# Optimization experiments

Measured on AMD Instinct MI355X. Metric: run time of the kernel, lower is better.

## Reference

```python
import jax, jax.numpy as jnp
import numpy as np

EMBED_DIM = 2048
N_HEADS = 16
N_KV_HEADS = 4
HEAD_DIM = EMBED_DIM // N_HEADS  # 128
NUM_REP = N_HEADS // N_KV_HEADS  # 4
BATCH = 4
SEQLEN = 2048


def setup_inputs() -> dict:
    key = jax.random.key(0)
    kx, kq, kk, kv, ko = jax.random.split(key, 5)
    x = jax.random.normal(kx, (BATCH, SEQLEN, EMBED_DIM), dtype=jnp.float32)
    # Real RoPE table (theta=10000), shape (seqlen, head_dim//2)
    inv_freq = 1.0 / (10000.0 ** (jnp.arange(0, HEAD_DIM, 2, dtype=jnp.float32) / HEAD_DIM))
    t = jnp.arange(SEQLEN, dtype=jnp.float32)
    ang = jnp.outer(t, inv_freq)  # (S, hd/2)
    freqs_cos = jnp.cos(ang)
    freqs_sin = jnp.sin(ang)
    std = 0.02
    wq = jax.random.normal(kq, (EMBED_DIM, N_HEADS * HEAD_DIM), dtype=jnp.float32) * std
    wk = jax.random.normal(kk, (EMBED_DIM, N_KV_HEADS * HEAD_DIM), dtype=jnp.float32) * std
    wv = jax.random.normal(kv, (EMBED_DIM, N_KV_HEADS * HEAD_DIM), dtype=jnp.float32) * std
    wo = jax.random.normal(ko, (N_HEADS * HEAD_DIM, EMBED_DIM), dtype=jnp.float32) * std
    return {"x": x, "freqs_cos": freqs_cos, "freqs_sin": freqs_sin,
            "wq": wq, "wk": wk, "wv": wv, "wo": wo}


def _apply_rope(xh, cos, sin):
    # xh: (b, s, h, hd); cos/sin: (s, hd/2) -> broadcast (1, s, 1, hd/2)
    b, s, h, hd = xh.shape
    xr = xh.reshape(b, s, h, hd // 2, 2)
    x0, x1 = xr[..., 0], xr[..., 1]  # real/imag of complex pairs
    c = cos[None, :, None, :]
    sn = sin[None, :, None, :]
    o0 = x0 * c - x1 * sn
    o1 = x0 * sn + x1 * c
    return jnp.stack([o0, o1], axis=-1).reshape(b, s, h, hd)


def reference(x, freqs_cos, freqs_sin, wq, wk, wv, wo):
    bs, s, _ = x.shape
    xq = (x @ wq).reshape(bs, s, N_HEADS, HEAD_DIM)
    xk = (x @ wk).reshape(bs, s, N_KV_HEADS, HEAD_DIM)
    xv = (x @ wv).reshape(bs, s, N_KV_HEADS, HEAD_DIM)
    xq = _apply_rope(xq, freqs_cos, freqs_sin)
    xk = _apply_rope(xk, freqs_cos, freqs_sin)
    # repeat_kv (GQA): interleave-repeat kv heads to match query heads
    keys = jnp.repeat(xk, NUM_REP, axis=2)    # (b, s, H, hd)
    values = jnp.repeat(xv, NUM_REP, axis=2)
    scale = 1.0 / jnp.sqrt(jnp.float32(HEAD_DIM))
    # SDPA, non-causal
    scores = jnp.einsum('bqhd,bkhd->bhqk', xq, keys) * scale
    probs = jax.nn.softmax(scores, axis=-1)
    out = jnp.einsum('bhqk,bkhd->bqhd', probs, values)
    out = out.reshape(bs, s, N_HEADS * HEAD_DIM)
    return out @ wo
```

## Files before the change

### kernel.cpp

```cpp
#include <hip/hip_runtime.h>
#include <stdint.h>


typedef unsigned short u16;
typedef __bf16 bf16x8 __attribute__((ext_vector_type(8)));
typedef float  f32x4  __attribute__((ext_vector_type(4)));
typedef unsigned int u32x2 __attribute__((ext_vector_type(2)));

#define GLOAD16(gp, lp)                                                        \
  __builtin_amdgcn_global_load_lds(                                            \
      (const __attribute__((address_space(1))) void*)(gp),                     \
      (__attribute__((address_space(3))) void*)(lp), 16, 0, 0)

__device__ __forceinline__ u16 f2b(float f) {
  union { float f; uint32_t u; } v; v.f = f;
  uint32_t r = v.u + 0x7FFFu + ((v.u >> 16) & 1u);
  return (u16)(r >> 16);
}
__device__ __forceinline__ float b2f(u16 h) {
  union { uint32_t u; float f; } v; v.u = ((uint32_t)h) << 16;
  return v.f;
}
__device__ __forceinline__ uint2 pack4(float a, float b, float c, float d) {
  uint2 r;
  asm("v_cvt_pk_bf16_f32 %0, %1, %2" : "=v"(r.x) : "v"(a), "v"(b));
  asm("v_cvt_pk_bf16_f32 %0, %1, %2" : "=v"(r.y) : "v"(c), "v"(d));
  return r;
}

__device__ __forceinline__ void bar_sync() {
  asm volatile("s_waitcnt lgkmcnt(0)" ::: "memory");
  __builtin_amdgcn_s_barrier();
  asm volatile("" ::: "memory");
}

__global__ __launch_bounds__(256) void cast_x_kernel(const float4* __restrict__ in,
                                                     ushort4* __restrict__ out) {
  int i = blockIdx.x * 256 + threadIdx.x;
  float4 v = in[i];
  ushort4 o;
  o.x = f2b(v.x); o.y = f2b(v.y); o.z = f2b(v.z); o.w = f2b(v.w);
  out[i] = o;
}

__global__ __launch_bounds__(256) void wtrans_kernel(const float* __restrict__ W,
                                                     u16* __restrict__ WT,
                                                     int K, int N, float scale) {
  __shared__ float t[32][33];
  int n0 = blockIdx.x * 32, k0 = blockIdx.y * 32;
  int tx = threadIdx.x, ty = threadIdx.y;
  for (int r = 0; r < 4; r++)
    t[ty + r * 8][tx] = W[(size_t)(k0 + ty + r * 8) * N + n0 + tx];
  __syncthreads();
  for (int r = 0; r < 4; r++)
    WT[(size_t)(n0 + ty + r * 8) * K + k0 + tx] = f2b(t[tx][ty + r * 8] * scale);
}

template <bool BF16OUT>
__global__ __launch_bounds__(256) void gemm_bt_kernel(const u16* __restrict__ A,
                                                      const u16* __restrict__ BT,
                                                      void* __restrict__ Cv,
                                                      int K, int N) {
  __shared__ u16 As[128 * 64];
  __shared__ u16 Bs[128 * 64];
  const int tid = threadIdx.x;
  const int wave = tid >> 6, lane = tid & 63;
  const int quad = lane >> 4, l16 = lane & 15;
  const int wm = (wave >> 1) * 64, wn = (wave & 1) * 64;
  const size_t m0 = (size_t)blockIdx.y * 128, n0 = (size_t)blockIdx.x * 128;

  f32x4 acc[4][4] = {};
  const int srow = lane >> 3;
  const int scol = ((lane & 7) ^ srow) * 8;
  const u16* Ag = A + (m0 + wave * 8 + srow) * (size_t)K + scol;
  const u16* Bg = BT + (n0 + wave * 8 + srow) * (size_t)K + scol;
  const int sw7 = l16 & 7;

  for (int k0 = 0; k0 < K; k0 += 64) {
    for (int c = 0; c < 4; c++) {
      GLOAD16(Ag + (size_t)(c * 32) * K + k0, &As[(c * 32 + wave * 8) * 64]);
      GLOAD16(Bg + (size_t)(c * 32) * K + k0, &Bs[(c * 32 + wave * 8) * 64]);
    }
    __syncthreads();
    for (int kk = 0; kk < 2; kk++) {
      bf16x8 af[4], bf[4];
      const int ch = ((4 * kk + quad) ^ sw7) << 3;
      for (int i = 0; i < 4; i++)
        af[i] = *(const bf16x8*)&As[(wm + i * 16 + l16) * 64 + ch];
      for (int i = 0; i < 4; i++)
        bf[i] = *(const bf16x8*)&Bs[(wn + i * 16 + l16) * 64 + ch];
      for (int mi = 0; mi < 4; mi++)
        for (int ni = 0; ni < 4; ni++)
          acc[mi][ni] = __builtin_amdgcn_mfma_f32_16x16x32_bf16(af[mi], bf[ni], acc[mi][ni], 0, 0, 0);
    }
    __syncthreads();
  }
  for (int mi = 0; mi < 4; mi++)
    for (int ni = 0; ni < 4; ni++)
      for (int r = 0; r < 4; r++) {
        size_t row = m0 + wm + mi * 16 + quad * 4 + r;
        size_t col = n0 + wn + ni * 16 + l16;
        if (BF16OUT) ((u16*)Cv)[row * N + col] = f2b(acc[mi][ni][r]);
        else         ((float*)Cv)[row * N + col] = acc[mi][ni][r];
      }
}

__global__ __launch_bounds__(256) void rope_kernel(u16* __restrict__ QKV,
                                                   const float* __restrict__ cs,
                                                   const float* __restrict__ sn) {
  int tid = blockIdx.x * 256 + threadIdx.x;
  int row = tid / 1280;
  int p = tid - row * 1280;
  int s = row & 2047;
  int head = p >> 6, i = p & 63;
  u16* ptr = QKV + (size_t)row * 3072 + head * 128 + i * 2;
  unsigned int v = *(unsigned int*)ptr;
  float x0 = b2f((u16)(v & 0xffff)), x1 = b2f((u16)(v >> 16));
  float c = cs[s * 64 + i], ss = sn[s * 64 + i];
  u16 o0 = f2b(x0 * c - x1 * ss);
  u16 o1 = f2b(x0 * ss + x1 * c);
  *(unsigned int*)ptr = (unsigned int)o0 | ((unsigned int)o1 << 16);
}

__global__ __launch_bounds__(256) void vtrans_kernel(const u16* __restrict__ QKV,
                                                     u16* __restrict__ Vt) {
  __shared__ u16 t[32][33];
  int b = blockIdx.z >> 2, hk = blockIdx.z & 3;
  int s0 = blockIdx.x * 32, d0 = blockIdx.y * 32;
  int tx = threadIdx.x, ty = threadIdx.y;
  const u16* src = QKV + (size_t)(b * 2048 + s0) * 3072 + 2560 + hk * 128 + d0;
  for (int r = 0; r < 4; r++)
    t[ty + r * 8][tx] = src[(size_t)(ty + r * 8) * 3072 + tx];
  __syncthreads();
  u16* dst = Vt + ((size_t)((b * 4 + hk) * 128 + d0)) * 2048 + s0;
  for (int r = 0; r < 4; r++)
    dst[(size_t)(ty + r * 8) * 2048 + tx] = t[tx][ty + r * 8];
}

__global__ __launch_bounds__(256, 2) void attn_kernel(const u16* __restrict__ QKV,
                                                      const u16* __restrict__ Vt,
                                                      u16* __restrict__ AO) {
  __shared__ u16 KP[128 * 128];
  __shared__ u16 Vls[128 * 128];
  const int tid = threadIdx.x;
  const int wave = tid >> 6, lane = tid & 63;
  const int quad = lane >> 4, l16 = lane & 15;
  const int qt = blockIdx.x, h = blockIdx.y, b = blockIdx.z;
  const int hk = h >> 2;
  const int sw = l16 & 7;

  bf16x8 qf[2][4];
  {
    const u16* Qb = QKV + (size_t)(b * 2048 + qt * 128 + wave * 32) * 3072 + h * 128;
    for (int qb = 0; qb < 2; qb++)
      for (int ki = 0; ki < 4; ki++)
        qf[qb][ki] = *(const bf16x8*)(Qb + (size_t)(qb * 16 + l16) * 3072 + ki * 32 + quad * 8);
  }
  f32x4 o[8][2] = {};
  float m_[2] = {-1e30f, -1e30f}, l_[2] = {0.f, 0.f};

  const u16* Kg0 = QKV + 2048 + hk * 128;
  const u16* Vg0 = Vt + (size_t)((b * 4 + hk) * 128) * 2048;
  const int r4 = lane >> 4, c16 = lane & 15;

  auto stageK = [&](int t) {
    const u16* Kg = Kg0 + (size_t)(b * 2048 + t * 128) * 3072;
    for (int i = 0; i < 8; i++) {
      int grp = i * 4 + wave;
      int row = grp * 4 + r4;
      int ch = c16 ^ (row & 7);
      GLOAD16(Kg + (size_t)row * 3072 + ch * 8, &KP[grp * 512]);
    }
  };
  auto stageV = [&](int t) {
    const u16* Vg = Vg0 + t * 128;
    for (int i = 0; i < 8; i++) {
      int grp = i * 4 + wave;
      int row = grp * 4 + r4;
      int ch = c16 ^ (row & 7);
      GLOAD16(Vg + (size_t)row * 2048 + ch * 8, &Vls[grp * 512]);
    }
  };

  stageK(0);
  stageV(0);
  __syncthreads();

  for (int kt = 0; kt < 16; kt++) {
    if (kt > 0) stageV(kt);

    f32x4 s[8][2];
    for (int kb = 0; kb < 8; kb++) {
      bf16x8 kf[4];
      int a0 = (kb * 16 + l16) * 128 + ((quad ^ sw) << 3);
      for (int ki = 0; ki < 4; ki++)
        kf[ki] = *(const bf16x8*)&KP[a0 ^ (ki * 32)];
      __builtin_amdgcn_s_setprio(1);
      for (int qb = 0; qb < 2; qb++) {
        f32x4 a = {0.f, 0.f, 0.f, 0.f};
        for (int ki = 0; ki < 4; ki++)
          a = __builtin_amdgcn_mfma_f32_16x16x32_bf16(kf[ki], qf[qb][ki], a, 0, 0, 0);
        s[kb][qb] = a;
      }
      __builtin_amdgcn_s_setprio(0);
    }

    bar_sync();
    if (kt < 15) stageK(kt + 1);

    bf16x8 pf[2][4];
    float alch[2];
    for (int qb = 0; qb < 2; qb++) {
      float mk[8];
#pragma unroll
      for (int kb = 0; kb < 8; kb++)
        mk[kb] = fmaxf(fmaxf(s[kb][qb][0], s[kb][qb][1]),
                       fmaxf(s[kb][qb][2], s[kb][qb][3]));
      float mx = fmaxf(fmaxf(fmaxf(mk[0], mk[1]), fmaxf(mk[2], mk[3])),
                       fmaxf(fmaxf(mk[4], mk[5]), fmaxf(mk[6], mk[7])));
      mx = fmaxf(mx, __shfl_xor(mx, 16, 64));
      mx = fmaxf(mx, __shfl_xor(mx, 32, 64));
      float mn = m_[qb], al = 1.0f;
      if (!__all(mx <= m_[qb] + 8.0f)) {
        mn = fmaxf(m_[qb], mx);
        al = exp2f(m_[qb] - mn);
        m_[qb] = mn;
      }
      alch[qb] = al;
      uint2 u[8];
      float rs = 0.f;
#pragma unroll
      for (int kb = 0; kb < 8; kb++) {
        float p0 = exp2f(s[kb][qb][0] - mn), p1 = exp2f(s[kb][qb][1] - mn);
        float p2 = exp2f(s[kb][qb][2] - mn), p3 = exp2f(s[kb][qb][3] - mn);
        u[kb] = pack4(p0, p1, p2, p3);
        rs += (p0 + p1) + (p2 + p3);
      }
      rs += __shfl_xor(rs, 16, 64);
      rs += __shfl_xor(rs, 32, 64);
      l_[qb] = l_[qb] * al + rs;
      const bool qo = (quad & 1) != 0;
#pragma unroll
      for (int ki = 0; ki < 4; ki++) {
        u32x2 r1 = __builtin_amdgcn_permlane32_swap(u[2 * ki].x, u[2 * ki + 1].x, false, false);
        u32x2 r2 = __builtin_amdgcn_permlane32_swap(u[2 * ki].y, u[2 * ki + 1].y, false, false);
        uint32_t t1b = (uint32_t)__shfl_xor((int)r1[1], 16, 64);
        uint32_t t1a = (uint32_t)__shfl_xor((int)r1[0], 16, 64);
        uint32_t t2b = (uint32_t)__shfl_xor((int)r2[1], 16, 64);
        uint32_t t2a = (uint32_t)__shfl_xor((int)r2[0], 16, 64);
        uint4 d;
        d.x = qo ? t1b : (uint32_t)r1[0];
        d.y = qo ? t2b : (uint32_t)r2[0];
        d.z = qo ? (uint32_t)r1[1] : t1a;
        d.w = qo ? (uint32_t)r2[1] : t2a;
        pf[qb][ki] = *(bf16x8*)&d;
      }
    }
    if (alch[0] != 1.0f || alch[1] != 1.0f) {
#pragma unroll
      for (int db = 0; db < 8; db++) {
        o[db][0] *= alch[0];
        o[db][1] *= alch[1];
      }
    }

    if (kt == 15) asm volatile("s_waitcnt vmcnt(0)" ::: "memory");
    else          asm volatile("s_waitcnt vmcnt(8)" ::: "memory");
    bar_sync();

    for (int db = 0; db < 8; db++) {
      bf16x8 vf[4];
      int a0 = (db * 16 + l16) * 128 + ((quad ^ sw) << 3);
      for (int ki = 0; ki < 4; ki++)
        vf[ki] = *(const bf16x8*)&Vls[a0 ^ (ki * 32)];
      __builtin_amdgcn_s_setprio(1);
      for (int qb = 0; qb < 2; qb++)
        for (int ki = 0; ki < 4; ki++)
          o[db][qb] = __builtin_amdgcn_mfma_f32_16x16x32_bf16(vf[ki], pf[qb][ki], o[db][qb], 0, 0, 0);
      __builtin_amdgcn_s_setprio(0);
    }

    asm volatile("s_waitcnt vmcnt(0)" ::: "memory");
    bar_sync();
  }

  float inv[2] = {1.0f / l_[0], 1.0f / l_[1]};
  for (int qb = 0; qb < 2; qb++) {
    int rq = wave * 32 + qb * 16 + l16;
    for (int db = 0; db < 8; db++) {
      int ch = (db * 2 + (quad >> 1)) ^ sw;
      uint2 pv = pack4(o[db][qb][0] * inv[qb], o[db][qb][1] * inv[qb],
                       o[db][qb][2] * inv[qb], o[db][qb][3] * inv[qb]);
      *(uint2*)&KP[rq * 128 + (ch << 3) + (quad & 1) * 4] = pv;
    }
  }
  __syncthreads();
  u16* Ab = AO + (size_t)(b * 2048 + qt * 128) * 2048 + h * 128;
  for (int i = 0; i < 8; i++) {
    int row = i * 16 + (tid >> 4);
    int seg = tid & 15;
    int pc = seg ^ (row & 7);
    *(uint4*)(Ab + (size_t)row * 2048 + seg * 8) = *(const uint4*)&KP[row * 128 + pc * 8];
  }
}

extern "C" void kernel_launch(void* const* d_in, const int* in_sizes, int n_in,
                              void* d_out, int out_size, void* d_ws, size_t ws_size,
                              hipStream_t stream) {
  (void)in_sizes; (void)n_in; (void)out_size; (void)ws_size;
  const float* x    = (const float*)d_in[0];
  const float* fcos = (const float*)d_in[1];
  const float* fsin = (const float*)d_in[2];
  const float* wq   = (const float*)d_in[3];
  const float* wk   = (const float*)d_in[4];
  const float* wv   = (const float*)d_in[5];
  const float* wo   = (const float*)d_in[6];

  char* w = (char*)d_ws;
  u16* xb  = (u16*)w;
  u16* wT  = (u16*)(w + 33554432);
  u16* woT = (u16*)(w + 33554432 + 12582912);
  u16* QKV = (u16*)(w + 33554432 + 12582912 + 8388608);
  u16* Vt  = (u16*)(w + 33554432 + 12582912 + 8388608 + 50331648);
  u16* AO  = xb;

  const float C = 0.08838834764831845f * 1.44269504088896340f;

  cast_x_kernel<<<16384, 256, 0, stream>>>((const float4*)x, (ushort4*)xb);
  wtrans_kernel<<<dim3(64, 64), dim3(32, 8), 0, stream>>>(wq, wT, 2048, 2048, C);
  wtrans_kernel<<<dim3(16, 64), dim3(32, 8), 0, stream>>>(wk, wT + (size_t)2048 * 2048, 2048, 512, 1.0f);
  wtrans_kernel<<<dim3(16, 64), dim3(32, 8), 0, stream>>>(wv, wT + (size_t)2560 * 2048, 2048, 512, 1.0f);
  wtrans_kernel<<<dim3(64, 64), dim3(32, 8), 0, stream>>>(wo, woT, 2048, 2048, 1.0f);

  gemm_bt_kernel<true><<<dim3(24, 64), 256, 0, stream>>>(xb, wT, QKV, 2048, 3072);
  rope_kernel<<<40960, 256, 0, stream>>>(QKV, fcos, fsin);
  vtrans_kernel<<<dim3(64, 4, 16), dim3(32, 8), 0, stream>>>(QKV, Vt);
  attn_kernel<<<dim3(16, 16, 4), 256, 0, stream>>>(QKV, Vt, AO);
  gemm_bt_kernel<false><<<dim3(16, 64), 256, 0, stream>>>(AO, woT, (float*)d_out, 2048, 2048);
}
```

Measured before the change: 575.7 us.

## Double-buffer GEMM LDS tiles and remap workgroups across XCDs

The GEMM main loop is rebuilt around K=32 steps with two LDS buffers, so the next tile's global-to-LDS loads are issued before the MFMAs on the current tile. This needs only one barrier per step instead of two. It uses a new swizzled LDS layout, and raises wave priority with s_setprio around the MFMA block. Both the GEMM and attention kernels now remap linear block IDs so that neighbouring tiles land on the same XCD, aiming to improve L2 reuse. The risks are added register pressure, smaller K tiles meaning more barriers overall, and reliance on a bar_sync helper defined elsewhere.

Result: no change. 573.1 us (-0.5%).

```diff
diff --git a/kernel.cpp b/kernel.cpp
--- a/kernel.cpp
+++ b/kernel.cpp
@@ -56,45 +56,68 @@
     WT[(size_t)(n0 + ty + r * 8) * K + k0 + tx] = f2b(t[tx][ty + r * 8] * scale);
 }
 
+#define KSTEP(CUR, NXT, TT)                                                    \
+  {                                                                            \
+    asm volatile("s_waitcnt vmcnt(0)" ::: "memory");                           \
+    bar_sync();                                                                \
+    if ((TT) + 1 < nt) {                                                       \
+      const size_t k0 = (size_t)((TT) + 1) * 32;                               \
+      GLOAD16(Ag + k0, &As[NXT][ldst]);                                        \
+      GLOAD16(Ag + k0 + (size_t)16 * K, &As[NXT][ldst + 512]);                 \
+      GLOAD16(Bg + k0, &Bs[NXT][ldst]);                                        \
+      GLOAD16(Bg + k0 + (size_t)16 * K, &Bs[NXT][ldst + 512]);                 \
+    }                                                                          \
+    bf16x8 af[4], bf[4];                                                       \
+    for (int i = 0; i < 4; i++)                                                \
+      af[i] = *(const bf16x8*)&As[CUR][wm * 32 + i * 512 + lrd];               \
+    for (int i = 0; i < 4; i++)                                                \
+      bf[i] = *(const bf16x8*)&Bs[CUR][wn * 32 + i * 512 + lrd];               \
+    __builtin_amdgcn_s_setprio(1);                                             \
+    for (int mi = 0; mi < 4; mi++)                                             \
+      for (int ni = 0; ni < 4; ni++)                                           \
+        acc[mi][ni] = __builtin_amdgcn_mfma_f32_16x16x32_bf16(                 \
+            af[mi], bf[ni], acc[mi][ni], 0, 0, 0);                             \
+    __builtin_amdgcn_s_setprio(0);                                             \
+  }
+
 template <bool BF16OUT>
 __global__ __launch_bounds__(256) void gemm_bt_kernel(const u16* __restrict__ A,
                                                       const u16* __restrict__ BT,
                                                       void* __restrict__ Cv,
                                                       int K, int N) {
-  __shared__ u16 As[128 * 64];
-  __shared__ u16 Bs[128 * 64];
+  __shared__ u16 As[2][64 * 64];
+  __shared__ u16 Bs[2][64 * 64];
   const int tid = threadIdx.x;
   const int wave = tid >> 6, lane = tid & 63;
   const int quad = lane >> 4, l16 = lane & 15;
   const int wm = (wave >> 1) * 64, wn = (wave & 1) * 64;
-  const size_t m0 = (size_t)blockIdx.y * 128, n0 = (size_t)blockIdx.x * 128;
+
+  const int nbx = gridDim.x;
+  const int nwg = nbx * gridDim.y;
+  const int d = blockIdx.x + blockIdx.y * nbx;
+  const int w = (d & 7) * (nwg >> 3) + (d >> 3);
+  const size_t m0 = (size_t)(w / nbx) * 128, n0 = (size_t)(w % nbx) * 128;
 
   f32x4 acc[4][4] = {};
-  const int srow = lane >> 3;
-  const int scol = ((lane & 7) ^ srow) * 8;
-  const u16* Ag = A + (m0 + wave * 8 + srow) * (size_t)K + scol;
-  const u16* Bg = BT + (n0 + wave * 8 + srow) * (size_t)K + scol;
-  const int sw7 = l16 & 7;
-
-  for (int k0 = 0; k0 < K; k0 += 64) {
-    for (int c = 0; c < 4; c++) {
-      GLOAD16(Ag + (size_t)(c * 32) * K + k0, &As[(c * 32 + wave * 8) * 64]);
-      GLOAD16(Bg + (size_t)(c * 32) * K + k0, &Bs[(c * 32 + wave * 8) * 64]);
-    }
-    __syncthreads();
-    for (int kk = 0; kk < 2; kk++) {
-      bf16x8 af[4], bf[4];
-      const int ch = ((4 * kk + quad) ^ sw7) << 3;
-      for (int i = 0; i < 4; i++)
-        af[i] = *(const bf16x8*)&As[(wm + i * 16 + l16) * 64 + ch];
-      for (int i = 0; i < 4; i++)
-        bf[i] = *(const bf16x8*)&Bs[(wn + i * 16 + l16) * 64 + ch];
-      for (int mi = 0; mi < 4; mi++)
-        for (int ni = 0; ni < 4; ni++)
-          acc[mi][ni] = __builtin_amdgcn_mfma_f32_16x16x32_bf16(af[mi], bf[ni], acc[mi][ni], 0, 0, 0);
-    }
-    __syncthreads();
-  }
+  const int srow = wave * 32 + ((lane >> 3) << 1) + ((lane >> 2) & 1);
+  const int tcol = ((lane & 3) ^ ((lane >> 3) & 3)) * 8;
+  const u16* Ag = A + (m0 + srow) * (size_t)K + tcol;
+  const u16* Bg = BT + (n0 + srow) * (size_t)K + tcol;
+  const int ldst = wave * 1024;
+  const int lrd = (l16 >> 1) * 64 + (l16 & 1) * 32 +
+                  ((quad ^ ((l16 >> 1) & 3)) << 3);
+  const int nt = K >> 5;
+
+  GLOAD16(Ag, &As[0][ldst]);
+  GLOAD16(Ag + (size_t)16 * K, &As[0][ldst + 512]);
+  GLOAD16(Bg, &Bs[0][ldst]);
+  GLOAD16(Bg + (size_t)16 * K, &Bs[0][ldst + 512]);
+
+  for (int t = 0; t < nt; t += 2) {
+    KSTEP(0, 1, t);
+    KSTEP(1, 0, t + 1);
+  }
+
   for (int mi = 0; mi < 4; mi++)
     for (int ni = 0; ni < 4; ni++)
       for (int r = 0; r < 4; r++) {
@@ -145,7 +168,9 @@
   const int tid = threadIdx.x;
   const int wave = tid >> 6, lane = tid & 63;
   const int quad = lane >> 4, l16 = lane & 15;
-  const int qt = blockIdx.x, h = blockIdx.y, b = blockIdx.z;
+  const int d0s = blockIdx.x + 16 * (blockIdx.y + 16 * blockIdx.z);
+  const int w0 = (d0s & 7) * 128 + (d0s >> 3);
+  const int qt = w0 & 15, h = (w0 >> 4) & 15, b = w0 >> 8;
   const int hk = h >> 2;
   const int sw = l16 & 7;
 
```

## Rewrite GEMM as 256x256 double-buffered pipelined kernel and fuse RoPE epilogue

Applied to the files above, without the earlier changes.

Replaces the 128x128 single-buffered GEMM with a 512-thread 256x256 tile kernel that double-buffers LDS across 128-wide K steps. Global-to-LDS loads are interleaved with MFMA phases using barriers, vmcnt waits and s_setprio, and workgroups are remapped in an XCD-aware order. RoPE is fused into the QKV GEMM epilogue using a lane shuffle to fetch the pair element, which drops the separate rope kernel and its extra pass over QKV. The cost is larger LDS use, one workgroup per CU, and fewer workgroups (384 and 256) to fill the device.

New measurement: 1.619 ms. +181.3%, slower.

```diff
diff --git a/kernel.cpp b/kernel.cpp
--- a/kernel.cpp
+++ b/kernel.cpp
@@ -56,70 +56,131 @@
     WT[(size_t)(n0 + ty + r * 8) * K + k0 + tx] = f2b(t[tx][ty + r * 8] * scale);
 }
 
+#define STG_A(T, KS)                                                           \
+  GLOAD16(PA + (size_t)(T) * 64 + (KS) * 32,                                   \
+          &SH[(((T) & 1) * 2 + (KS)) * 8192 + ldw]);                           \
+  GLOAD16(PA + (size_t)128 * K + (size_t)(T) * 64 + (KS) * 32,                 \
+          &SH[(((T) & 1) * 2 + (KS)) * 8192 + ldw + 4096]);
+
+#define STG_B(T, KS)                                                           \
+  GLOAD16(PB + (size_t)(T) * 64 + (KS) * 32,                                   \
+          &SH[32768 + (((T) & 1) * 2 + (KS)) * 8192 + ldw]);                   \
+  GLOAD16(PB + (size_t)128 * K + (size_t)(T) * 64 + (KS) * 32,                 \
+          &SH[32768 + (((T) & 1) * 2 + (KS)) * 8192 + ldw + 4096]);
+
+#define PHASE(TP, KS, MH, STAGE_STMT, WAIT_STMT)                               \
+  {                                                                            \
+    bf16x8 af[4];                                                              \
+    const int ao = ((TP) * 2 + (KS)) * 8192;                                   \
+    for (int q = 0; q < 4; q++)                                                \
+      af[q] = *(const bf16x8*)&SH[ao + aBase + ((MH) * 4 + q) * 512];          \
+    if ((MH) == 0)                                                             \
+      for (int q = 0; q < 4; q++)                                              \
+        bf[q] = *(const bf16x8*)&SH[32768 + ao + bBase + q * 512];             \
+    STAGE_STMT;                                                                \
+    __builtin_amdgcn_s_barrier();                                              \
+    asm volatile("s_waitcnt lgkmcnt(0)" ::: "memory");                         \
+    __builtin_amdgcn_s_setprio(1);                                             \
+    for (int q = 0; q < 4; q++)                                                \
+      for (int nr = 0; nr < 4; nr++)                                           \
+        acc[(MH) * 4 + q][nr] = __builtin_amdgcn_mfma_f32_16x16x32_bf16(       \
+            af[q], bf[nr], acc[(MH) * 4 + q][nr], 0, 0, 0);                    \
+    __builtin_amdgcn_s_setprio(0);                                             \
+    WAIT_STMT;                                                                 \
+    __builtin_amdgcn_s_barrier();                                              \
+    asm volatile("" ::: "memory");                                             \
+  }
+
 template <bool BF16OUT>
-__global__ __launch_bounds__(256) void gemm_bt_kernel(const u16* __restrict__ A,
-                                                      const u16* __restrict__ BT,
-                                                      void* __restrict__ Cv,
-                                                      int K, int N) {
-  __shared__ u16 As[128 * 64];
-  __shared__ u16 Bs[128 * 64];
+__global__ __launch_bounds__(512, 1) void gemm_bt_kernel(const u16* __restrict__ A,
+                                                         const u16* __restrict__ BT,
+                                                         void* __restrict__ Cv,
+                                                         int K, int N,
+                                                         const float* __restrict__ cs,
+                                                         const float* __restrict__ sn) {
+  __shared__ u16 SH[65536];
   const int tid = threadIdx.x;
   const int wave = tid >> 6, lane = tid & 63;
   const int quad = lane >> 4, l16 = lane & 15;
-  const int wm = (wave >> 1) * 64, wn = (wave & 1) * 64;
-  const size_t m0 = (size_t)blockIdx.y * 128, n0 = (size_t)blockIdx.x * 128;
-
-  f32x4 acc[4][4] = {};
-  const int srow = lane >> 3;
-  const int scol = ((lane & 7) ^ srow) * 8;
-  const u16* Ag = A + (m0 + wave * 8 + srow) * (size_t)K + scol;
-  const u16* Bg = BT + (n0 + wave * 8 + srow) * (size_t)K + scol;
-  const int sw7 = l16 & 7;
-
-  for (int k0 = 0; k0 < K; k0 += 64) {
-    for (int c = 0; c < 4; c++) {
-      GLOAD16(Ag + (size_t)(c * 32) * K + k0, &As[(c * 32 + wave * 8) * 64]);
-      GLOAD16(Bg + (size_t)(c * 32) * K + k0, &Bs[(c * 32 + wave * 8) * 64]);
-    }
-    __syncthreads();
-    for (int kk = 0; kk < 2; kk++) {
-      bf16x8 af[4], bf[4];
-      const int ch = ((4 * kk + quad) ^ sw7) << 3;
-      for (int i = 0; i < 4; i++)
-        af[i] = *(const bf16x8*)&As[(wm + i * 16 + l16) * 64 + ch];
-      for (int i = 0; i < 4; i++)
-        bf[i] = *(const bf16x8*)&Bs[(wn + i * 16 + l16) * 64 + ch];
-      for (int mi = 0; mi < 4; mi++)
-        for (int ni = 0; ni < 4; ni++)
-          acc[mi][ni] = __builtin_amdgcn_mfma_f32_16x16x32_bf16(af[mi], bf[ni], acc[mi][ni], 0, 0, 0);
-    }
-    __syncthreads();
-  }
-  for (int mi = 0; mi < 4; mi++)
-    for (int ni = 0; ni < 4; ni++)
-      for (int r = 0; r < 4; r++) {
-        size_t row = m0 + wm + mi * 16 + quad * 4 + r;
-        size_t col = n0 + wn + ni * 16 + l16;
-        if (BF16OUT) ((u16*)Cv)[row * N + col] = f2b(acc[mi][ni][r]);
-        else         ((float*)Cv)[row * N + col] = acc[mi][ni][r];
-      }
-}
-
-__global__ __launch_bounds__(256) void rope_kernel(u16* __restrict__ QKV,
-                                                   const float* __restrict__ cs,
-                                                   const float* __restrict__ sn) {
-  int tid = blockIdx.x * 256 + threadIdx.x;
-  int row = tid / 1280;
-  int p = tid - row * 1280;
-  int s = row & 2047;
-  int head = p >> 6, i = p & 63;
-  u16* ptr = QKV + (size_t)row * 3072 + head * 128 + i * 2;
-  unsigned int v = *(unsigned int*)ptr;
-  float x0 = b2f((u16)(v & 0xffff)), x1 = b2f((u16)(v >> 16));
-  float c = cs[s * 64 + i], ss = sn[s * 64 + i];
-  u16 o0 = f2b(x0 * c - x1 * ss);
-  u16 o1 = f2b(x0 * ss + x1 * c);
-  *(unsigned int*)ptr = (unsigned int)o0 | ((unsigned int)o1 << 16);
+  const int wr = wave >> 2, wc = wave & 3;
+
+  const int nbx = gridDim.x;
+  const int nwg = nbx * gridDim.y;
+  const int d = blockIdx.x + blockIdx.y * nbx;
+  const int w = (d & 7) * (nwg >> 3) + (d >> 3);
+  const size_t m0 = (size_t)(w / nbx) * 256, n0 = (size_t)(w % nbx) * 256;
+
+  f32x4 acc[8][4] = {};
+
+  const int csw = ((lane & 3) ^ ((lane >> 2) & 3)) * 8;
+  const u16* PA = A + (m0 + wave * 16 + (lane >> 2)) * (size_t)K + csw;
+  const u16* PB = BT + (n0 + wave * 16 + (lane >> 2)) * (size_t)K + csw;
+  const int slot8 = (quad ^ (l16 & 3)) << 3;
+  const int aBase = (wr * 128 + l16) * 32 + slot8;
+  const int bBase = (wc * 64 + l16) * 32 + slot8;
+  const int ldw = wave * 512;
+
+  const int niter = K >> 7;
+
+  STG_A(0, 0) STG_A(0, 1) STG_B(0, 0) STG_B(0, 1)
+  STG_A(1, 0) STG_A(1, 1) STG_B(1, 0) STG_B(1, 1)
+  __syncthreads();
+
+  for (int i = 0; i < niter; i++) {
+    const int t0 = 2 * i;
+    const bool nx = (i + 1 < niter);
+    const bool p0 = (i > 0);
+    bf16x8 bf[4];
+    PHASE(0, 0, 0, if (p0) { STG_A(t0 + 1, 1) }, )
+    PHASE(0, 0, 1, if (p0) { STG_B(t0 + 1, 1) }, )
+    PHASE(0, 1, 0, if (nx) { STG_A(t0 + 2, 0) }, )
+    PHASE(0, 1, 1, if (nx) { STG_B(t0 + 2, 0) },
+          if (nx) { asm volatile("s_waitcnt vmcnt(4)" ::: "memory"); }
+          else    { asm volatile("s_waitcnt vmcnt(0)" ::: "memory"); })
+    PHASE(1, 0, 0, if (nx) { STG_A(t0 + 2, 1) }, )
+    PHASE(1, 0, 1, if (nx) { STG_B(t0 + 2, 1) }, )
+    PHASE(1, 1, 0, if (nx) { STG_A(t0 + 3, 0) }, )
+    PHASE(1, 1, 1, if (nx) { STG_B(t0 + 3, 0) },
+          if (nx) { asm volatile("s_waitcnt vmcnt(4)" ::: "memory"); }
+          else    { asm volatile("s_waitcnt vmcnt(0)" ::: "memory"); })
+  }
+
+  if constexpr (BF16OUT) {
+    if ((int)n0 >= 2560) {
+      for (int mr = 0; mr < 8; mr++)
+        for (int nr = 0; nr < 4; nr++)
+          for (int r = 0; r < 4; r++) {
+            size_t row = m0 + wr * 128 + mr * 16 + quad * 4 + r;
+            size_t col = n0 + wc * 64 + nr * 16 + l16;
+            ((u16*)Cv)[row * N + col] = f2b(acc[mr][nr][r]);
+          }
+    } else {
+      for (int mr = 0; mr < 8; mr++)
+        for (int nr = 0; nr < 4; nr++) {
+          int col = (int)n0 + wc * 64 + nr * 16 + l16;
+          int ii = (col & 127) >> 1;
+          bool odd = (col & 1) != 0;
+          for (int r = 0; r < 4; r++) {
+            int row = (int)m0 + wr * 128 + mr * 16 + quad * 4 + r;
+            int s = row & 2047;
+            float v = acc[mr][nr][r];
+            float pv = __shfl_xor(v, 1, 64);
+            float c_ = cs[(size_t)s * 64 + ii];
+            float s_ = sn[(size_t)s * 64 + ii];
+            float out = odd ? (pv * s_ + v * c_) : (v * c_ - pv * s_);
+            ((u16*)Cv)[(size_t)row * N + col] = f2b(out);
+          }
+        }
+    }
+  } else {
+    for (int mr = 0; mr < 8; mr++)
+      for (int nr = 0; nr < 4; nr++)
+        for (int r = 0; r < 4; r++) {
+          size_t row = m0 + wr * 128 + mr * 16 + quad * 4 + r;
+          size_t col = n0 + wc * 64 + nr * 16 + l16;
+          ((float*)Cv)[row * N + col] = acc[mr][nr][r];
+        }
+  }
 }
 
 __global__ __launch_bounds__(256) void vtrans_kernel(const u16* __restrict__ QKV,
@@ -332,9 +393,10 @@
   wtrans_kernel<<<dim3(16, 64), dim3(32, 8), 0, stream>>>(wv, wT + (size_t)2560 * 2048, 2048, 512, 1.0f);
   wtrans_kernel<<<dim3(64, 64), dim3(32, 8), 0, stream>>>(wo, woT, 2048, 2048, 1.0f);
 
-  gemm_bt_kernel<true><<<dim3(24, 64), 256, 0, stream>>>(xb, wT, QKV, 2048, 3072);
-  rope_kernel<<<40960, 256, 0, stream>>>(QKV, fcos, fsin);
+  gemm_bt_kernel<true><<<dim3(12, 32), 512, 0, stream>>>(xb, wT, QKV, 2048, 3072,
+                                                         fcos, fsin);
   vtrans_kernel<<<dim3(64, 4, 16), dim3(32, 8), 0, stream>>>(QKV, Vt);
   attn_kernel<<<dim3(16, 16, 4), 256, 0, stream>>>(QKV, Vt, AO);
-  gemm_bt_kernel<false><<<dim3(16, 64), 256, 0, stream>>>(AO, woT, (float*)d_out, 2048, 2048);
-}
+  gemm_bt_kernel<false><<<dim3(8, 32), 512, 0, stream>>>(AO, woT, (float*)d_out, 2048, 2048,
+                                                         nullptr, nullptr);
+}
```
